# Kernel optimization log

Hardware: AMD Instinct MI355X
Metric: run time of the kernel (lower is better)

Reference implementation:

```python
import jax, jax.numpy as jnp
import numpy as np

B, N, D, H = 4, 4096, 1024, 16
HD = D // H  # 64
EPS_NORM = 1e-12  # F.normalize eps
EPS_LN = 1e-5     # layernorm eps


def setup_inputs() -> dict:
    key = jax.random.key(0)
    ks = jax.random.split(key, 9)
    s = 0.02
    return {
        "x": jax.random.normal(ks[0], (B, N, D), jnp.float32),
        "Wq": jax.random.normal(ks[1], (D, D), jnp.float32) * s,
        "Wk": jax.random.normal(ks[2], (D, D), jnp.float32) * s,
        "Wv": jax.random.normal(ks[3], (D, D), jnp.float32) * s,
        "Wf": jax.random.normal(ks[4], (H, D), jnp.float32) * s,
        "Wg1": jax.random.normal(ks[5], (HD, D), jnp.float32) * s,
        "Wg2": jax.random.normal(ks[6], (D, HD), jnp.float32) * s,
        "ln_w": jnp.ones((D,), jnp.float32),
        "Wo": jax.random.normal(ks[7], (D, D), jnp.float32) * s,
    }


def _silu(x):
    return x * jax.nn.sigmoid(x)


def _simple_gla(q, k, v, f):
    # q,k,v: [B,N,H,HD], f: [B,N,H] log-decay. Recurrence:
    #   S_t = exp(f_t) * S_{t-1} + k_t v_t^T ;  o_t = q_t^T S_t  (scale=1)
    qT = jnp.moveaxis(q, 1, 0)  # [N,B,H,HD]
    kT = jnp.moveaxis(k, 1, 0)
    vT = jnp.moveaxis(v, 1, 0)
    fT = jnp.moveaxis(f, 1, 0)  # [N,B,H]

    def step(S, inp):
        qt, kt, vt, ft = inp
        S = jnp.exp(ft)[..., None, None] * S + kt[..., :, None] * vt[..., None, :]
        o = jnp.einsum('bhk,bhkv->bhv', qt, S)
        return S, o

    S0 = jnp.zeros((q.shape[0], q.shape[2], q.shape[3], v.shape[3]), q.dtype)
    _, o = jax.lax.scan(step, S0, (qT, kT, vT, fT))
    return jnp.moveaxis(o, 0, 1)  # [B,N,H,HD]


def reference(x, Wq, Wk, Wv, Wf, Wg1, Wg2, ln_w, Wo):
    b, n, d = x.shape
    q = _silu(x @ Wq.T).reshape(b, n, H, HD)
    k = _silu(x @ Wk.T).reshape(b, n, H, HD)
    v = _silu(x @ Wv.T).reshape(b, n, H, HD)
    f = jax.nn.log_sigmoid(x @ Wf.T)  # [B,N,H] scalar per-head log decay
    # F.normalize(k, p=2, dim=-1)
    k = k / jnp.maximum(jnp.linalg.norm(k, axis=-1, keepdims=True), EPS_NORM)

    o = _simple_gla(q, k, v, f).reshape(b, n, d)

    # output gate: sigmoid(Linear(d->hd) -> Linear(hd->d))
    gate = jax.nn.sigmoid((x @ Wg1.T) @ Wg2.T)
    o = o * gate

    # layernorm without bias
    mu = jnp.mean(o, axis=-1, keepdims=True)
    xc = o - mu
    var = jnp.mean(xc * xc, axis=-1, keepdims=True)
    o = xc / jnp.sqrt(var + EPS_LN) * ln_w

    return o @ Wo.T
```

## Files before the change

### kernel.cpp

```cpp
#include <hip/hip_runtime.h>
#include <stdint.h>


#define NWIDE 3200

typedef __attribute__((ext_vector_type(4))) float f32x4;
typedef __attribute__((ext_vector_type(4))) unsigned short u16x4;
typedef __attribute__((ext_vector_type(8))) unsigned short u16x8;
typedef __attribute__((ext_vector_type(8))) __bf16 bf16x8;

__device__ __forceinline__ float bf2f(unsigned short u) {
    union { unsigned int i; float f; } c; c.i = ((unsigned int)u) << 16; return c.f;
}
__device__ __forceinline__ unsigned short f2bf(float f) {
    union { float f; unsigned int i; } c; c.f = f;
    return (unsigned short)((c.i + 0x7fffu + ((c.i >> 16) & 1u)) >> 16);
}
__device__ __forceinline__ float siluf(float x) { return x / (1.f + __expf(-x)); }
__device__ __forceinline__ float logsigf(float z) {
    return (z >= 0.f) ? -log1pf(__expf(-z)) : (z - log1pf(__expf(z)));
}
__device__ __forceinline__ f32x4 MFMA(bf16x8 a, bf16x8 b, f32x4 c) {
    return __builtin_amdgcn_mfma_f32_16x16x32_bf16(a, b, c, 0, 0, 0);
}
__device__ __forceinline__ void lds16(const void* g, void* l) {
    __builtin_amdgcn_global_load_lds(
        (const __attribute__((address_space(1))) unsigned int*)(uintptr_t)g,
        (__attribute__((address_space(3))) unsigned int*)(unsigned int)(uintptr_t)l,
        16, 0, 0);
}

__global__ __launch_bounds__(256) void k_convert(const float* __restrict__ src,
                                                 unsigned short* __restrict__ dst, int n4) {
    int i = blockIdx.x * 256 + threadIdx.x;
    if (i >= n4) return;
    f32x4 v = ((const f32x4*)src)[i];
    u16x4 o;
#pragma unroll
    for (int e = 0; e < 4; e++) o[e] = f2bf(v[e]);
    ((u16x4*)dst)[i] = o;
}

__global__ __launch_bounds__(256) void k_wcat(const float* __restrict__ Wq, const float* __restrict__ Wk,
                                              const float* __restrict__ Wv, const float* __restrict__ Wf,
                                              const float* __restrict__ Wg1, unsigned short* __restrict__ Wcat) {
    const int r = blockIdx.x, t = threadIdx.x;
    const float* src = nullptr; int sr = r;
    if (r < 1024) { src = Wq; }
    else if (r < 2048) { src = Wk; sr = r - 1024; }
    else if (r < 3072) { src = Wv; sr = r - 2048; }
    else if (r < 3088) { src = Wf; sr = r - 3072; }
    else if (r < 3152) { src = Wg1; sr = r - 3088; }
    u16x4 o;
    if (src) {
        f32x4 v = *(const f32x4*)&src[(size_t)sr * 1024 + 4 * t];
#pragma unroll
        for (int e = 0; e < 4; e++) o[e] = f2bf(v[e]);
    } else {
        o[0] = 0; o[1] = 0; o[2] = 0; o[3] = 0;
    }
    *(u16x4*)&Wcat[(size_t)r * 1024 + 4 * t] = o;
}

template <int MODE>
__global__ __launch_bounds__(256)
void k_gemm(const unsigned short* __restrict__ A, const unsigned short* __restrict__ Bw,
            void* __restrict__ outp, float* __restrict__ fbuf, int M, int N, int K, int ldOut) {
    __shared__ __align__(16) unsigned short As[128 * 32];
    __shared__ __align__(16) unsigned short Bs[128 * 32];
    const int tid = threadIdx.x;
    const int w = tid >> 6, lane = tid & 63;
    const int cpx = gridDim.x >> 3;
    const int mt = (blockIdx.x & 7) * cpx + (blockIdx.x >> 3);
    const int m0 = mt * 128, n0 = blockIdx.y * 128;
    const int srow = lane >> 2, scol = (lane & 3) * 8;
    const int fr = lane & 15, fg = lane >> 4;
    const int wr = w >> 1, wc = w & 1;
    f32x4 acc[4][4] = {};
    const int kc = K >> 5;
    for (int kt = 0; kt < kc; ++kt) {
        const int k0 = kt << 5;
        __syncthreads();
        {
            const unsigned short* ga = A + (size_t)(m0 + 32 * w + srow) * K + k0 + scol;
            lds16(ga, &As[(32 * w) * 32]);
            const unsigned short* ga2 = A + (size_t)(m0 + 32 * w + 16 + srow) * K + k0 + scol;
            lds16(ga2, &As[(32 * w + 16) * 32]);
            const unsigned short* gb = Bw + (size_t)(n0 + 32 * w + srow) * K + k0 + scol;
            lds16(gb, &Bs[(32 * w) * 32]);
            const unsigned short* gb2 = Bw + (size_t)(n0 + 32 * w + 16 + srow) * K + k0 + scol;
            lds16(gb2, &Bs[(32 * w + 16) * 32]);
        }
        __syncthreads();
        bf16x8 av[4], bv[4];
#pragma unroll
        for (int i = 0; i < 4; i++) av[i] = *(const bf16x8*)&As[(64 * wr + 16 * i + fr) * 32 + fg * 8];
#pragma unroll
        for (int j = 0; j < 4; j++) bv[j] = *(const bf16x8*)&Bs[(64 * wc + 16 * j + fr) * 32 + fg * 8];
#pragma unroll
        for (int i = 0; i < 4; i++)
#pragma unroll
            for (int j = 0; j < 4; j++)
                acc[i][j] = MFMA(av[i], bv[j], acc[i][j]);
    }
    const int nb = n0 + 64 * wc;
    if (MODE == 1) {
        float* O = (float*)outp;
#pragma unroll
        for (int i = 0; i < 4; i++)
#pragma unroll
            for (int j = 0; j < 4; j++) {
                const int gc = nb + 16 * j + fr;
#pragma unroll
                for (int r = 0; r < 4; r++)
                    O[(size_t)(m0 + 64 * wr + 16 * i + 4 * fg + r) * ldOut + gc] = acc[i][j][r];
            }
        return;
    }
    unsigned short* Y = (unsigned short*)outp;
    if (nb >= 3072) {
#pragma unroll
        for (int i = 0; i < 4; i++)
#pragma unroll
            for (int j = 0; j < 4; j++) {
                const int gc = nb + 16 * j + fr;
#pragma unroll
                for (int r = 0; r < 4; r++) {
                    const int gr = m0 + 64 * wr + 16 * i + 4 * fg + r;
                    const float v = acc[i][j][r];
                    if (gc < 3088) {
                        if (gc >= 3072) fbuf[gr * 16 + (gc - 3072)] = logsigf(v);
                    } else if (gc < 3152) {
                        Y[(size_t)gr * ldOut + gc] = f2bf(v);
                    }
                }
            }
    } else if (nb >= 1024 && nb < 2048) {
#pragma unroll
        for (int i = 0; i < 4; i++)
#pragma unroll
            for (int j = 0; j < 4; j++)
#pragma unroll
                for (int r = 0; r < 4; r++) acc[i][j][r] = siluf(acc[i][j][r]);
#pragma unroll
        for (int i = 0; i < 4; i++)
#pragma unroll
            for (int r = 0; r < 4; r++) {
                float ss = 0.f;
#pragma unroll
                for (int j = 0; j < 4; j++) ss += acc[i][j][r] * acc[i][j][r];
                ss += __shfl_xor(ss, 1, 64);
                ss += __shfl_xor(ss, 2, 64);
                ss += __shfl_xor(ss, 4, 64);
                ss += __shfl_xor(ss, 8, 64);
                const float sc = 1.f / fmaxf(sqrtf(ss), 1e-12f);
                const int gr = m0 + 64 * wr + 16 * i + 4 * fg + r;
#pragma unroll
                for (int j = 0; j < 4; j++)
                    Y[(size_t)gr * ldOut + nb + 16 * j + fr] = f2bf(acc[i][j][r] * sc);
            }
    } else {
#pragma unroll
        for (int i = 0; i < 4; i++)
#pragma unroll
            for (int j = 0; j < 4; j++) {
                const int gc = nb + 16 * j + fr;
#pragma unroll
                for (int r = 0; r < 4; r++)
                    Y[(size_t)(m0 + 64 * wr + 16 * i + 4 * fg + r) * ldOut + gc] = f2bf(siluf(acc[i][j][r]));
            }
    }
}

__global__ void k_cumsum(const float* __restrict__ fbuf, float* __restrict__ cbuf) {
    const int cid = blockIdx.x, t = threadIdx.x;
    const int bh = cid >> 6, ic = cid & 63;
    const int b = bh >> 4, h = bh & 15;
    float v = fbuf[(size_t)(b * 4096 + ic * 64 + t) * 16 + h];
#pragma unroll
    for (int off = 1; off < 64; off <<= 1) {
        float u = __shfl_up(v, (unsigned)off, 64);
        if (t >= off) v += u;
    }
    cbuf[(size_t)cid * 64 + t] = v;
}

__global__ __launch_bounds__(256)
void k_chunk_kv(const unsigned short* __restrict__ Y, const float* __restrict__ cbuf,
                unsigned short* __restrict__ St) {
    __shared__ __align__(16) unsigned short Kt[64 * 72];
    __shared__ __align__(16) unsigned short Vt[64 * 72];
    __shared__ float cs[64];
    const int cid = blockIdx.x, tid = threadIdx.x;
    const int bh = cid >> 6, ic = cid & 63;
    const int b = bh >> 4, h = bh & 15;
    if (tid < 64) cs[tid] = cbuf[(size_t)cid * 64 + tid];
    __syncthreads();
    const int s = tid >> 2, c0 = (tid & 3) << 4;
    const float wdec = __expf(cs[63] - cs[s]);
    const size_t rowg = (size_t)(b * 4096 + ic * 64 + s) * NWIDE;
    u16x8 k0v = *(const u16x8*)&Y[rowg + 1024 + h * 64 + c0];
    u16x8 k1v = *(const u16x8*)&Y[rowg + 1024 + h * 64 + c0 + 8];
    u16x8 v0v = *(const u16x8*)&Y[rowg + 2048 + h * 64 + c0];
    u16x8 v1v = *(const u16x8*)&Y[rowg + 2048 + h * 64 + c0 + 8];
#pragma unroll
    for (int e = 0; e < 8; e++) {
        Kt[(c0 + e) * 72 + s] = f2bf(bf2f(k0v[e]) * wdec);
        Kt[(c0 + 8 + e) * 72 + s] = f2bf(bf2f(k1v[e]) * wdec);
        Vt[(c0 + e) * 72 + s] = v0v[e];
        Vt[(c0 + 8 + e) * 72 + s] = v1v[e];
    }
    __syncthreads();
    const int w = tid >> 6, lane = tid & 63;
    const int fr = lane & 15, fg = lane >> 4;
    f32x4 acc[4] = {};
#pragma unroll
    for (int ks = 0; ks < 2; ks++) {
        bf16x8 a = *(const bf16x8*)&Kt[(16 * w + fr) * 72 + ks * 32 + fg * 8];
#pragma unroll
        for (int j = 0; j < 4; j++)
            acc[j] = MFMA(a, *(const bf16x8*)&Vt[(16 * j + fr) * 72 + ks * 32 + fg * 8], acc[j]);
    }
    unsigned short* outp = St + (size_t)cid * 4096;
#pragma unroll
    for (int j = 0; j < 4; j++)
#pragma unroll
        for (int r = 0; r < 4; r++)
            outp[(16 * w + 4 * fg + r) * 64 + 16 * j + fr] = f2bf(acc[j][r]);
}

__global__ void k_scan(unsigned short* __restrict__ St, const float* __restrict__ cbuf) {
    const int bh = blockIdx.x >> 4;
    const int e = ((blockIdx.x & 15) << 8) + threadIdx.x;
    float S = 0.f;
    const size_t base = (size_t)bh * 64 * 4096 + e;
    for (int i = 0; i < 64; i++) {
        const float d = __expf(cbuf[(bh * 64 + i) * 64 + 63]);
        const float m = bf2f(St[base + (size_t)i * 4096]);
        St[base + (size_t)i * 4096] = f2bf(S);
        S = d * S + m;
    }
}

__global__ __launch_bounds__(256)
void k_chunk_out(const unsigned short* __restrict__ Y, const float* __restrict__ cbuf,
                 const unsigned short* __restrict__ St, const unsigned short* __restrict__ Wg2b,
                 unsigned short* __restrict__ og) {
    __shared__ __align__(16) unsigned short Qs[64 * 72];
    __shared__ __align__(16) unsigned short Ks[64 * 72];
    __shared__ __align__(16) unsigned short Vt[64 * 72];
    __shared__ __align__(16) unsigned short S0[64 * 72];
    __shared__ __align__(16) unsigned short G1[64 * 72];
    __shared__ __align__(16) unsigned short W2[64 * 72];
    __shared__ __align__(16) unsigned short Pl[4 * 16 * 72];
    __shared__ float cs[64];
    const int cid = blockIdx.x, tid = threadIdx.x;
    const int bh = cid >> 6, ic = cid & 63;
    const int b = bh >> 4, h = bh & 15;
    if (tid < 64) cs[tid] = cbuf[(size_t)cid * 64 + tid];
    const int s = tid >> 2, c0 = (tid & 3) << 4;
    const size_t rowg = (size_t)(b * 4096 + ic * 64 + s) * NWIDE;
    *(u16x8*)&Qs[s * 72 + c0] = *(const u16x8*)&Y[rowg + h * 64 + c0];
    *(u16x8*)&Qs[s * 72 + c0 + 8] = *(const u16x8*)&Y[rowg + h * 64 + c0 + 8];
    *(u16x8*)&Ks[s * 72 + c0] = *(const u16x8*)&Y[rowg + 1024 + h * 64 + c0];
    *(u16x8*)&Ks[s * 72 + c0 + 8] = *(const u16x8*)&Y[rowg + 1024 + h * 64 + c0 + 8];
    *(u16x8*)&G1[s * 72 + c0] = *(const u16x8*)&Y[rowg + 3088 + c0];
    *(u16x8*)&G1[s * 72 + c0 + 8] = *(const u16x8*)&Y[rowg + 3088 + c0 + 8];
    *(u16x8*)&W2[s * 72 + c0] = *(const u16x8*)&Wg2b[(size_t)(h * 64 + s) * 64 + c0];
    *(u16x8*)&W2[s * 72 + c0 + 8] = *(const u16x8*)&Wg2b[(size_t)(h * 64 + s) * 64 + c0 + 8];
    {
        u16x8 v0v = *(const u16x8*)&Y[rowg + 2048 + h * 64 + c0];
        u16x8 v1v = *(const u16x8*)&Y[rowg + 2048 + h * 64 + c0 + 8];
        u16x8 s0v = *(const u16x8*)&St[(size_t)cid * 4096 + s * 64 + c0];
        u16x8 s1v = *(const u16x8*)&St[(size_t)cid * 4096 + s * 64 + c0 + 8];
#pragma unroll
        for (int e = 0; e < 8; e++) {
            Vt[(c0 + e) * 72 + s] = v0v[e];
            Vt[(c0 + 8 + e) * 72 + s] = v1v[e];
            S0[(c0 + e) * 72 + s] = s0v[e];
            S0[(c0 + 8 + e) * 72 + s] = s1v[e];
        }
    }
    __syncthreads();
    const int w = tid >> 6, lane = tid & 63;
    const int fr = lane & 15, fg = lane >> 4;
    bf16x8 aq[2];
#pragma unroll
    for (int ks = 0; ks < 2; ks++) aq[ks] = *(const bf16x8*)&Qs[(16 * w + fr) * 72 + ks * 32 + fg * 8];
    f32x4 sc[4] = {};
#pragma unroll
    for (int ks = 0; ks < 2; ks++)
#pragma unroll
        for (int j = 0; j < 4; j++)
            sc[j] = MFMA(aq[ks], *(const bf16x8*)&Ks[(16 * j + fr) * 72 + ks * 32 + fg * 8], sc[j]);
    const int tl = 16 * w + 4 * fg;
#pragma unroll
    for (int j = 0; j < 4; j++)
#pragma unroll
        for (int r = 0; r < 4; r++) {
            const int tt = tl + r, ss2 = 16 * j + fr;
            float p = (ss2 <= tt) ? sc[j][r] * __expf(cs[tt] - cs[ss2]) : 0.f;
            Pl[w * (16 * 72) + (4 * fg + r) * 72 + ss2] = f2bf(p);
        }
    __syncthreads();
    f32x4 ov[4] = {};
#pragma unroll
    for (int ks = 0; ks < 2; ks++) {
        bf16x8 ap = *(const bf16x8*)&Pl[w * (16 * 72) + fr * 72 + ks * 32 + fg * 8];
#pragma unroll
        for (int j = 0; j < 4; j++)
            ov[j] = MFMA(ap, *(const bf16x8*)&Vt[(16 * j + fr) * 72 + ks * 32 + fg * 8], ov[j]);
    }
    f32x4 qs[4] = {};
#pragma unroll
    for (int ks = 0; ks < 2; ks++)
#pragma unroll
        for (int j = 0; j < 4; j++)
            qs[j] = MFMA(aq[ks], *(const bf16x8*)&S0[(16 * j + fr) * 72 + ks * 32 + fg * 8], qs[j]);
    bf16x8 ag[2];
#pragma unroll
    for (int ks = 0; ks < 2; ks++) ag[ks] = *(const bf16x8*)&G1[(16 * w + fr) * 72 + ks * 32 + fg * 8];
    f32x4 gl[4] = {};
#pragma unroll
    for (int ks = 0; ks < 2; ks++)
#pragma unroll
        for (int j = 0; j < 4; j++)
            gl[j] = MFMA(ag[ks], *(const bf16x8*)&W2[(16 * j + fr) * 72 + ks * 32 + fg * 8], gl[j]);
#pragma unroll
    for (int j = 0; j < 4; j++)
#pragma unroll
        for (int r = 0; r < 4; r++) {
            const int tt = tl + r;
            const float o = ov[j][r] + __expf(cs[tt]) * qs[j][r];
            const float g = 1.f / (1.f + __expf(-gl[j][r]));
            og[(size_t)(b * 4096 + ic * 64 + tt) * 1024 + h * 64 + 16 * j + fr] = f2bf(o * g);
        }
}

__global__ __launch_bounds__(256)
void k_ln(unsigned short* __restrict__ og, const float* __restrict__ lnw) {
    __shared__ float red[8];
    const int r = blockIdx.x, t = threadIdx.x;
    unsigned short* p = og + (size_t)r * 1024;
    u16x4 a = *(u16x4*)&p[4 * t];
    float x[4]; float s = 0.f, ssum = 0.f;
#pragma unroll
    for (int e = 0; e < 4; e++) { x[e] = bf2f(a[e]); s += x[e]; ssum += x[e] * x[e]; }
#pragma unroll
    for (int m = 1; m < 64; m <<= 1) { s += __shfl_xor(s, m, 64); ssum += __shfl_xor(ssum, m, 64); }
    const int w = t >> 6;
    if ((t & 63) == 0) { red[w] = s; red[4 + w] = ssum; }
    __syncthreads();
    s = red[0] + red[1] + red[2] + red[3];
    ssum = red[4] + red[5] + red[6] + red[7];
    const float mu = s * (1.f / 1024.f);
    const float var = ssum * (1.f / 1024.f) - mu * mu;
    const float rs = rsqrtf(var + 1e-5f);
    u16x4 o;
#pragma unroll
    for (int e = 0; e < 4; e++) o[e] = f2bf((x[e] - mu) * rs * lnw[4 * t + e]);
    *(u16x4*)&p[4 * t] = o;
}

extern "C" void kernel_launch(void* const* d_in, const int* in_sizes, int n_in,
                              void* d_out, int out_size, void* d_ws, size_t ws_size,
                              hipStream_t stream) {
    const float* x = (const float*)d_in[0];
    const float* Wq = (const float*)d_in[1];
    const float* Wk = (const float*)d_in[2];
    const float* Wv = (const float*)d_in[3];
    const float* Wf = (const float*)d_in[4];
    const float* Wg1 = (const float*)d_in[5];
    const float* Wg2 = (const float*)d_in[6];
    const float* lnw = (const float*)d_in[7];
    const float* Wo = (const float*)d_in[8];
    char* ws = (char*)d_ws;
    unsigned short* xb = (unsigned short*)(ws + 0);
    unsigned short* Yb = (unsigned short*)(ws + 33554432LL);
    unsigned short* Wcat = (unsigned short*)(ws + 138412032LL);
    unsigned short* Wob = (unsigned short*)(ws + 144965632LL);
    unsigned short* Wg2b = (unsigned short*)(ws + 147062784LL);
    float* fbuf = (float*)(ws + 147193856LL);
    float* cbuf = (float*)(ws + 148242432LL);
    unsigned short* St = (unsigned short*)(ws + 149291008LL);
    unsigned short* og = xb;

    k_convert<<<16384, 256, 0, stream>>>(x, xb, 4194304);
    k_wcat<<<3200, 256, 0, stream>>>(Wq, Wk, Wv, Wf, Wg1, Wcat);
    k_convert<<<1024, 256, 0, stream>>>(Wo, Wob, 262144);
    k_convert<<<64, 256, 0, stream>>>(Wg2, Wg2b, 16384);
    k_gemm<0><<<dim3(128, 25), 256, 0, stream>>>(xb, Wcat, Yb, fbuf, 16384, 3200, 1024, 3200);
    k_cumsum<<<4096, 64, 0, stream>>>(fbuf, cbuf);
    k_chunk_kv<<<4096, 256, 0, stream>>>(Yb, cbuf, St);
    k_scan<<<1024, 256, 0, stream>>>(St, cbuf);
    k_chunk_out<<<4096, 256, 0, stream>>>(Yb, cbuf, St, Wg2b, og);
    k_ln<<<16384, 256, 0, stream>>>(og, lnw);
    k_gemm<1><<<dim3(128, 8), 256, 0, stream>>>(og, Wob, d_out, nullptr, 16384, 1024, 1024, 1024);
}
```

Baseline: 355.8 us.

## Move SiLU, key normalization and logsigmoid from GEMM epilogue into consumer kernels

```diff
diff --git a/kernel.cpp b/kernel.cpp
--- a/kernel.cpp
+++ b/kernel.cpp
@@ -65,14 +65,12 @@
 template <int MODE>
 __global__ __launch_bounds__(256)
 void k_gemm(const unsigned short* __restrict__ A, const unsigned short* __restrict__ Bw,
-            void* __restrict__ outp, float* __restrict__ fbuf, int M, int N, int K, int ldOut) {
+            void* __restrict__ outp, float* __restrict__ zbuf, int M, int N, int K, int ldOut) {
     __shared__ __align__(16) unsigned short As[128 * 32];
     __shared__ __align__(16) unsigned short Bs[128 * 32];
     const int tid = threadIdx.x;
     const int w = tid >> 6, lane = tid & 63;
-    const int cpx = gridDim.x >> 3;
-    const int mt = (blockIdx.x & 7) * cpx + (blockIdx.x >> 3);
-    const int m0 = mt * 128, n0 = blockIdx.y * 128;
+    const int m0 = blockIdx.x * 128, n0 = blockIdx.y * 128;
     const int srow = lane >> 2, scol = (lane & 3) * 8;
     const int fr = lane & 15, fg = lane >> 4;
     const int wr = w >> 1, wc = w & 1;
@@ -129,36 +127,12 @@
                     const int gr = m0 + 64 * wr + 16 * i + 4 * fg + r;
                     const float v = acc[i][j][r];
                     if (gc < 3088) {
-                        if (gc >= 3072) fbuf[gr * 16 + (gc - 3072)] = logsigf(v);
+                        if (gc >= 3072) zbuf[gr * 16 + (gc - 3072)] = v;
                     } else if (gc < 3152) {
                         Y[(size_t)gr * ldOut + gc] = f2bf(v);
                     }
                 }
             }
-    } else if (nb >= 1024 && nb < 2048) {
-#pragma unroll
-        for (int i = 0; i < 4; i++)
-#pragma unroll
-            for (int j = 0; j < 4; j++)
-#pragma unroll
-                for (int r = 0; r < 4; r++) acc[i][j][r] = siluf(acc[i][j][r]);
-#pragma unroll
-        for (int i = 0; i < 4; i++)
-#pragma unroll
-            for (int r = 0; r < 4; r++) {
-                float ss = 0.f;
-#pragma unroll
-                for (int j = 0; j < 4; j++) ss += acc[i][j][r] * acc[i][j][r];
-                ss += __shfl_xor(ss, 1, 64);
-                ss += __shfl_xor(ss, 2, 64);
-                ss += __shfl_xor(ss, 4, 64);
-                ss += __shfl_xor(ss, 8, 64);
-                const float sc = 1.f / fmaxf(sqrtf(ss), 1e-12f);
-                const int gr = m0 + 64 * wr + 16 * i + 4 * fg + r;
-#pragma unroll
-                for (int j = 0; j < 4; j++)
-                    Y[(size_t)gr * ldOut + nb + 16 * j + fr] = f2bf(acc[i][j][r] * sc);
-            }
     } else {
 #pragma unroll
         for (int i = 0; i < 4; i++)
@@ -167,16 +141,16 @@
                 const int gc = nb + 16 * j + fr;
 #pragma unroll
                 for (int r = 0; r < 4; r++)
-                    Y[(size_t)(m0 + 64 * wr + 16 * i + 4 * fg + r) * ldOut + gc] = f2bf(siluf(acc[i][j][r]));
+                    Y[(size_t)(m0 + 64 * wr + 16 * i + 4 * fg + r) * ldOut + gc] = f2bf(acc[i][j][r]);
             }
     }
 }
 
-__global__ void k_cumsum(const float* __restrict__ fbuf, float* __restrict__ cbuf) {
+__global__ void k_cumsum(const float* __restrict__ zbuf, float* __restrict__ cbuf) {
     const int cid = blockIdx.x, t = threadIdx.x;
     const int bh = cid >> 6, ic = cid & 63;
     const int b = bh >> 4, h = bh & 15;
-    float v = fbuf[(size_t)(b * 4096 + ic * 64 + t) * 16 + h];
+    float v = logsigf(zbuf[(size_t)(b * 4096 + ic * 64 + t) * 16 + h]);
 #pragma unroll
     for (int off = 1; off < 64; off <<= 1) {
         float u = __shfl_up(v, (unsigned)off, 64);
@@ -203,12 +177,20 @@
     u16x8 k1v = *(const u16x8*)&Y[rowg + 1024 + h * 64 + c0 + 8];
     u16x8 v0v = *(const u16x8*)&Y[rowg + 2048 + h * 64 + c0];
     u16x8 v1v = *(const u16x8*)&Y[rowg + 2048 + h * 64 + c0 + 8];
+    float kf[16]; float ss = 0.f;
+#pragma unroll
+    for (int e = 0; e < 8; e++) { kf[e] = siluf(bf2f(k0v[e])); ss += kf[e] * kf[e]; }
+#pragma unroll
+    for (int e = 0; e < 8; e++) { kf[8 + e] = siluf(bf2f(k1v[e])); ss += kf[8 + e] * kf[8 + e]; }
+    ss += __shfl_xor(ss, 1, 64);
+    ss += __shfl_xor(ss, 2, 64);
+    const float sc = wdec / fmaxf(sqrtf(ss), 1e-12f);
 #pragma unroll
     for (int e = 0; e < 8; e++) {
-        Kt[(c0 + e) * 72 + s] = f2bf(bf2f(k0v[e]) * wdec);
-        Kt[(c0 + 8 + e) * 72 + s] = f2bf(bf2f(k1v[e]) * wdec);
-        Vt[(c0 + e) * 72 + s] = v0v[e];
-        Vt[(c0 + 8 + e) * 72 + s] = v1v[e];
+        Kt[(c0 + e) * 72 + s] = f2bf(kf[e] * sc);
+        Kt[(c0 + 8 + e) * 72 + s] = f2bf(kf[8 + e] * sc);
+        Vt[(c0 + e) * 72 + s] = f2bf(siluf(bf2f(v0v[e])));
+        Vt[(c0 + 8 + e) * 72 + s] = f2bf(siluf(bf2f(v1v[e])));
     }
     __syncthreads();
     const int w = tid >> 6, lane = tid & 63;
@@ -260,10 +242,32 @@
     if (tid < 64) cs[tid] = cbuf[(size_t)cid * 64 + tid];
     const int s = tid >> 2, c0 = (tid & 3) << 4;
     const size_t rowg = (size_t)(b * 4096 + ic * 64 + s) * NWIDE;
-    *(u16x8*)&Qs[s * 72 + c0] = *(const u16x8*)&Y[rowg + h * 64 + c0];
-    *(u16x8*)&Qs[s * 72 + c0 + 8] = *(const u16x8*)&Y[rowg + h * 64 + c0 + 8];
-    *(u16x8*)&Ks[s * 72 + c0] = *(const u16x8*)&Y[rowg + 1024 + h * 64 + c0];
-    *(u16x8*)&Ks[s * 72 + c0 + 8] = *(const u16x8*)&Y[rowg + 1024 + h * 64 + c0 + 8];
+    {
+        u16x8 q0 = *(const u16x8*)&Y[rowg + h * 64 + c0];
+        u16x8 q1 = *(const u16x8*)&Y[rowg + h * 64 + c0 + 8];
+        u16x8 o0, o1;
+#pragma unroll
+        for (int e = 0; e < 8; e++) { o0[e] = f2bf(siluf(bf2f(q0[e]))); o1[e] = f2bf(siluf(bf2f(q1[e]))); }
+        *(u16x8*)&Qs[s * 72 + c0] = o0;
+        *(u16x8*)&Qs[s * 72 + c0 + 8] = o1;
+    }
+    {
+        u16x8 k0v = *(const u16x8*)&Y[rowg + 1024 + h * 64 + c0];
+        u16x8 k1v = *(const u16x8*)&Y[rowg + 1024 + h * 64 + c0 + 8];
+        float kf[16]; float ssn = 0.f;
+#pragma unroll
+        for (int e = 0; e < 8; e++) { kf[e] = siluf(bf2f(k0v[e])); ssn += kf[e] * kf[e]; }
+#pragma unroll
+        for (int e = 0; e < 8; e++) { kf[8 + e] = siluf(bf2f(k1v[e])); ssn += kf[8 + e] * kf[8 + e]; }
+        ssn += __shfl_xor(ssn, 1, 64);
+        ssn += __shfl_xor(ssn, 2, 64);
+        const float scn = 1.f / fmaxf(sqrtf(ssn), 1e-12f);
+        u16x8 o0, o1;
+#pragma unroll
+        for (int e = 0; e < 8; e++) { o0[e] = f2bf(kf[e] * scn); o1[e] = f2bf(kf[8 + e] * scn); }
+        *(u16x8*)&Ks[s * 72 + c0] = o0;
+        *(u16x8*)&Ks[s * 72 + c0 + 8] = o1;
+    }
     *(u16x8*)&G1[s * 72 + c0] = *(const u16x8*)&Y[rowg + 3088 + c0];
     *(u16x8*)&G1[s * 72 + c0 + 8] = *(const u16x8*)&Y[rowg + 3088 + c0 + 8];
     *(u16x8*)&W2[s * 72 + c0] = *(const u16x8*)&Wg2b[(size_t)(h * 64 + s) * 64 + c0];
@@ -275,8 +279,8 @@
         u16x8 s1v = *(const u16x8*)&St[(size_t)cid * 4096 + s * 64 + c0 + 8];
 #pragma unroll
         for (int e = 0; e < 8; e++) {
-            Vt[(c0 + e) * 72 + s] = v0v[e];
-            Vt[(c0 + 8 + e) * 72 + s] = v1v[e];
+            Vt[(c0 + e) * 72 + s] = f2bf(siluf(bf2f(v0v[e])));
+            Vt[(c0 + 8 + e) * 72 + s] = f2bf(siluf(bf2f(v1v[e])));
             S0[(c0 + e) * 72 + s] = s0v[e];
             S0[(c0 + 8 + e) * 72 + s] = s1v[e];
         }
@@ -380,7 +384,7 @@
     unsigned short* Wcat = (unsigned short*)(ws + 138412032LL);
     unsigned short* Wob = (unsigned short*)(ws + 144965632LL);
     unsigned short* Wg2b = (unsigned short*)(ws + 147062784LL);
-    float* fbuf = (float*)(ws + 147193856LL);
+    float* zbuf = (float*)(ws + 147193856LL);
     float* cbuf = (float*)(ws + 148242432LL);
     unsigned short* St = (unsigned short*)(ws + 149291008LL);
     unsigned short* og = xb;
@@ -389,8 +393,8 @@
     k_wcat<<<3200, 256, 0, stream>>>(Wq, Wk, Wv, Wf, Wg1, Wcat);
     k_convert<<<1024, 256, 0, stream>>>(Wo, Wob, 262144);
     k_convert<<<64, 256, 0, stream>>>(Wg2, Wg2b, 16384);
-    k_gemm<0><<<dim3(128, 25), 256, 0, stream>>>(xb, Wcat, Yb, fbuf, 16384, 3200, 1024, 3200);
-    k_cumsum<<<4096, 64, 0, stream>>>(fbuf, cbuf);
+    k_gemm<0><<<dim3(128, 25), 256, 0, stream>>>(xb, Wcat, Yb, zbuf, 16384, 3200, 1024, 3200);
+    k_cumsum<<<4096, 64, 0, stream>>>(zbuf, cbuf);
     k_chunk_kv<<<4096, 256, 0, stream>>>(Yb, cbuf, St);
     k_scan<<<1024, 256, 0, stream>>>(St, cbuf);
     k_chunk_out<<<4096, 256, 0, stream>>>(Yb, cbuf, St, Wg2b, og);
```

New measurement: 348.4 us. -2.1%, faster.
